# Kernel optimization log

Measured on AMD Instinct MI355X. Metric: run time of the kernel, lower is better.

## Reference

```python
import jax, jax.numpy as jnp
from jax import lax
import numpy as np

# sym6 reconstruction low-pass (pywt Wavelet('sym6').filter_bank[2]), length 12
SYM6_REC = [-0.007800708325034148, 0.0017677118642428036, 0.04472490177066578,
            -0.021060292512300564, -0.07263752278646252, 0.3379294217276218,
            0.787641141030194, 0.4910559419267466, -0.048311742585633,
            -0.11799011114819057, 0.0034907120842174702, 0.015404109327027373]

UP, DOWN = 1, 2
PAD = (len(SYM6_REC) - UP) // 2  # = 5


def setup_inputs() -> dict:
    key = jax.random.key(0)
    h = jnp.asarray(SYM6_REC, dtype=jnp.float32)
    kernel = h[None, :] * h[:, None]  # [12, 12] separable outer product
    x = jax.random.normal(key, (16, 64, 256, 256), dtype=jnp.float32)
    return {"input": x, "kernel": kernel}


def reference(input, kernel):
    # upfirdn2d: zero-insert upsample (lhs_dilation), pad, FIR convolve
    # (true convolution => flip kernel for lax correlation), strided downsample.
    B, C, H, W = input.shape
    w = jnp.flip(kernel, (0, 1))[None, None]        # [1, 1, kh, kw]
    x = input.reshape(B * C, 1, H, W)               # depthwise via batch fold
    y = lax.conv_general_dilated(
        x, w,
        window_strides=(DOWN, DOWN),
        padding=[(PAD, PAD), (PAD, PAD)],
        lhs_dilation=(UP, UP),
        dimension_numbers=('NCHW', 'OIHW', 'NCHW'))
    return y.reshape(B, C, y.shape[-2], y.shape[-1])
```

## Files before the change

kernel.cpp:

```cpp
#include <hip/hip_runtime.h>


#define H_IN  256
#define W_IN  256
#define H_OUT 128
#define W_OUT 128
#define KTAP  12
#define OTR   32
#define OTC   64
#define VSTR  148
#define NTHR  192

typedef float f32x4 __attribute__((ext_vector_type(4)));

__global__ __launch_bounds__(NTHR)
void upfirdn2d_sym6(const float* __restrict__ x,
                    const float* __restrict__ k2d,
                    float* __restrict__ out) {
    __shared__ float vs[OTR * VSTR];
    __shared__ float ks[KTAP * KTAP];
    __shared__ float wsh[KTAP];

    const int tid = threadIdx.x;

    if (tid < KTAP * KTAP) ks[tid] = k2d[tid];
    __syncthreads();
    if (tid < KTAP) {
        float tot = 0.f;
        #pragma unroll
        for (int i = 0; i < KTAP * KTAP; ++i) tot += ks[i];
        float rs = 0.f;
        #pragma unroll
        for (int q = 0; q < KTAP; ++q) rs += ks[(KTAP - 1 - tid) * KTAP + q];
        wsh[tid] = rs * rsqrtf(tot);
    }
    __syncthreads();
    float w[KTAP];
    #pragma unroll
    for (int p = 0; p < KTAP; ++p) w[p] = wsh[p];

    const int img = blockIdx.y;
    const int ti  = blockIdx.x >> 1;
    const int tj  = blockIdx.x & 1;
    const float* xim = x + (size_t)img * (H_IN * W_IN);

    const int gc0 = 128 * tj - 8;
    const bool edge_rows = (ti == 0) || (ti == 3);

    if (tid < 144) {
        const int rg  = tid / 36;
        const int cg  = tid - rg * 36;
        const int col = gc0 + 4 * cg;
        const bool colok = (unsigned)col < (unsigned)W_IN;
        const int i0  = rg * 8;
        const int gr0 = 64 * ti + 16 * rg - 5;

        float4 acc[8];
        #pragma unroll
        for (int k = 0; k < 8; ++k) acc[k] = make_float4(0.f, 0.f, 0.f, 0.f);

        if (!edge_rows) {
            const float* rp = xim + (size_t)gr0 * W_IN + col;
            #pragma unroll
            for (int rr = 0; rr < 26; ++rr) {
                float4 v = make_float4(0.f, 0.f, 0.f, 0.f);
                if (colok) v = *reinterpret_cast<const float4*>(rp);
                rp += W_IN;
                #pragma unroll
                for (int ri = 0; ri < 8; ++ri) {
                    const int p = rr - 2 * ri;
                    if (p >= 0 && p < KTAP) {
                        acc[ri].x = fmaf(w[p], v.x, acc[ri].x);
                        acc[ri].y = fmaf(w[p], v.y, acc[ri].y);
                        acc[ri].z = fmaf(w[p], v.z, acc[ri].z);
                        acc[ri].w = fmaf(w[p], v.w, acc[ri].w);
                    }
                }
            }
        } else {
            #pragma unroll
            for (int rr = 0; rr < 26; ++rr) {
                const int gr = gr0 + rr;
                float4 v = make_float4(0.f, 0.f, 0.f, 0.f);
                if (colok && (unsigned)gr < (unsigned)H_IN)
                    v = *reinterpret_cast<const float4*>(xim + gr * W_IN + col);
                #pragma unroll
                for (int ri = 0; ri < 8; ++ri) {
                    const int p = rr - 2 * ri;
                    if (p >= 0 && p < KTAP) {
                        acc[ri].x = fmaf(w[p], v.x, acc[ri].x);
                        acc[ri].y = fmaf(w[p], v.y, acc[ri].y);
                        acc[ri].z = fmaf(w[p], v.z, acc[ri].z);
                        acc[ri].w = fmaf(w[p], v.w, acc[ri].w);
                    }
                }
            }
        }
        #pragma unroll
        for (int ri = 0; ri < 8; ++ri)
            *reinterpret_cast<float4*>(&vs[(i0 + ri) * VSTR + 4 * cg]) = acc[ri];
    }
    __syncthreads();

    float* oim = out + (size_t)img * (H_OUT * W_OUT);
    for (int t = tid; t < 256; t += NTHR) {
        const int i = t >> 3;
        const int g = t & 7;

        float f[32];
        #pragma unroll
        for (int m = 0; m < 8; ++m) {
            float4 v4 = *reinterpret_cast<const float4*>(&vs[i * VSTR + 16 * g + 4 * m]);
            f[4*m+0] = v4.x; f[4*m+1] = v4.y; f[4*m+2] = v4.z; f[4*m+3] = v4.w;
        }
        float o[8];
        #pragma unroll
        for (int jj = 0; jj < 8; ++jj) {
            float a = 0.f;
            #pragma unroll
            for (int q = 0; q < KTAP; ++q)
                a = fmaf(w[q], f[2*jj + 3 + q], a);
            o[jj] = a;
        }
        const int orow = ti * OTR + i;
        const int ocol = tj * OTC + 8 * g;
        f32x4 o0 = { o[0], o[1], o[2], o[3] };
        f32x4 o1 = { o[4], o[5], o[6], o[7] };
        __builtin_nontemporal_store(o0, reinterpret_cast<f32x4*>(oim + orow * W_OUT + ocol));
        __builtin_nontemporal_store(o1, reinterpret_cast<f32x4*>(oim + orow * W_OUT + ocol + 4));
    }
}

extern "C" void kernel_launch(void* const* d_in, const int* in_sizes, int n_in,
                              void* d_out, int out_size, void* d_ws, size_t ws_size,
                              hipStream_t stream) {
    const float* x   = (const float*)d_in[0];
    const float* k2d = (const float*)d_in[1];
    float* out       = (float*)d_out;

    dim3 grid(8, 1024);
    dim3 block(NTHR);
    upfirdn2d_sym6<<<grid, block, 0, stream>>>(x, k2d, out);
}
```

Measured before the change: 70.95 us.

## Process two row tiles per block with double-buffered LDS overlap

Each block now handles two vertically adjacent 32-row output tiles, halving the grid. The second tile's vertical pass runs before the first tile's horizontal pass, using two LDS buffers, so global loads can overlap with the shuffle-and-FMA work. This amortizes the per-block kernel-weight setup, but doubles LDS per block, which may reduce occupancy. The kernel is already close to memory-bound.

Result: no change. 69.95 us, median of 2 (-1.4%).

```diff
diff --git a/kernel.cpp b/kernel.cpp
--- a/kernel.cpp
+++ b/kernel.cpp
@@ -7,59 +7,29 @@
 #define W_OUT 128
 #define KTAP  12
 #define OTR   32
-#define OTC   64
 #define VSTR  148
 #define NTHR  192
 
 typedef float f32x4 __attribute__((ext_vector_type(4)));
 
-__global__ __launch_bounds__(NTHR)
-void upfirdn2d_sym6(const float* __restrict__ x,
-                    const float* __restrict__ k2d,
-                    float* __restrict__ out) {
-    __shared__ float vs[OTR * VSTR];
-    __shared__ float ks[KTAP * KTAP];
-    __shared__ float wsh[KTAP];
-
-    const int tid = threadIdx.x;
-
-    if (tid < KTAP * KTAP) ks[tid] = k2d[tid];
-    __syncthreads();
-    if (tid < KTAP) {
-        float tot = 0.f;
-        #pragma unroll
-        for (int i = 0; i < KTAP * KTAP; ++i) tot += ks[i];
-        float rs = 0.f;
-        #pragma unroll
-        for (int q = 0; q < KTAP; ++q) rs += ks[(KTAP - 1 - tid) * KTAP + q];
-        wsh[tid] = rs * rsqrtf(tot);
-    }
-    __syncthreads();
-    float w[KTAP];
-    #pragma unroll
-    for (int p = 0; p < KTAP; ++p) w[p] = wsh[p];
-
-    const int img = blockIdx.y;
-    const int ti  = blockIdx.x >> 1;
-    const int tj  = blockIdx.x & 1;
-    const float* xim = x + (size_t)img * (H_IN * W_IN);
-
-    const int gc0 = 128 * tj - 8;
-    const bool edge_rows = (ti == 0) || (ti == 3);
-
+__device__ __forceinline__ void vpass(const float* __restrict__ xim,
+                                      float* __restrict__ buf,
+                                      const float (&w)[KTAP],
+                                      int tid, int b ,
+                                      int gc0, bool edge) {
     if (tid < 144) {
         const int rg  = tid / 36;
         const int cg  = tid - rg * 36;
         const int col = gc0 + 4 * cg;
         const bool colok = (unsigned)col < (unsigned)W_IN;
         const int i0  = rg * 8;
-        const int gr0 = 64 * ti + 16 * rg - 5;
+        const int gr0 = 2 * (b + i0) - 5;
 
         float4 acc[8];
         #pragma unroll
         for (int k = 0; k < 8; ++k) acc[k] = make_float4(0.f, 0.f, 0.f, 0.f);
 
-        if (!edge_rows) {
+        if (!edge) {
             const float* rp = xim + (size_t)gr0 * W_IN + col;
             #pragma unroll
             for (int rr = 0; rr < 26; ++rr) {
@@ -98,11 +68,14 @@
         }
         #pragma unroll
         for (int ri = 0; ri < 8; ++ri)
-            *reinterpret_cast<float4*>(&vs[(i0 + ri) * VSTR + 4 * cg]) = acc[ri];
+            *reinterpret_cast<float4*>(&buf[(i0 + ri) * VSTR + 4 * cg]) = acc[ri];
     }
-    __syncthreads();
+}
 
-    float* oim = out + (size_t)img * (H_OUT * W_OUT);
+__device__ __forceinline__ void hpass(const float* __restrict__ buf,
+                                      const float (&w)[KTAP],
+                                      float* __restrict__ oim,
+                                      int tid, int b, int ocol0) {
     for (int t = tid; t < 256; t += NTHR) {
         const int i = t >> 3;
         const int g = t & 7;
@@ -110,7 +83,7 @@
         float f[32];
         #pragma unroll
         for (int m = 0; m < 8; ++m) {
-            float4 v4 = *reinterpret_cast<const float4*>(&vs[i * VSTR + 16 * g + 4 * m]);
+            float4 v4 = *reinterpret_cast<const float4*>(&buf[i * VSTR + 16 * g + 4 * m]);
             f[4*m+0] = v4.x; f[4*m+1] = v4.y; f[4*m+2] = v4.z; f[4*m+3] = v4.w;
         }
         float o[8];
@@ -122,13 +95,59 @@
                 a = fmaf(w[q], f[2*jj + 3 + q], a);
             o[jj] = a;
         }
-        const int orow = ti * OTR + i;
-        const int ocol = tj * OTC + 8 * g;
         f32x4 o0 = { o[0], o[1], o[2], o[3] };
         f32x4 o1 = { o[4], o[5], o[6], o[7] };
-        __builtin_nontemporal_store(o0, reinterpret_cast<f32x4*>(oim + orow * W_OUT + ocol));
-        __builtin_nontemporal_store(o1, reinterpret_cast<f32x4*>(oim + orow * W_OUT + ocol + 4));
+        float* dst = oim + (size_t)(b + i) * W_OUT + ocol0 + 8 * g;
+        __builtin_nontemporal_store(o0, reinterpret_cast<f32x4*>(dst));
+        __builtin_nontemporal_store(o1, reinterpret_cast<f32x4*>(dst + 4));
     }
+}
+
+__global__ __launch_bounds__(NTHR)
+void upfirdn2d_sym6(const float* __restrict__ x,
+                    const float* __restrict__ k2d,
+                    float* __restrict__ out) {
+    __shared__ float vs[2][OTR * VSTR];
+    __shared__ float ks[KTAP * KTAP];
+    __shared__ float wsh[KTAP];
+
+    const int tid = threadIdx.x;
+
+    if (tid < KTAP * KTAP) ks[tid] = k2d[tid];
+    __syncthreads();
+    if (tid < KTAP) {
+        float tot = 0.f;
+        #pragma unroll
+        for (int i = 0; i < KTAP * KTAP; ++i) tot += ks[i];
+        float rs = 0.f;
+        #pragma unroll
+        for (int q = 0; q < KTAP; ++q) rs += ks[(KTAP - 1 - tid) * KTAP + q];
+        wsh[tid] = rs * rsqrtf(tot);
+    }
+    __syncthreads();
+    float w[KTAP];
+    #pragma unroll
+    for (int p = 0; p < KTAP; ++p) w[p] = wsh[p];
+
+    const int img = blockIdx.y;
+    const int ti  = blockIdx.x >> 1;
+    const int tj  = blockIdx.x & 1;
+    const float* xim = x + (size_t)img * (H_IN * W_IN);
+    float* oim = out + (size_t)img * (H_OUT * W_OUT);
+
+    const int gc0 = 128 * tj - 8;
+    const int b0  = 64 * ti;
+    const int b1  = 64 * ti + 32;
+    const bool e0 = (ti == 0);
+    const bool e1 = (ti == 1);
+    const int ocol0 = 64 * tj;
+
+    vpass(xim, vs[0], w, tid, b0, gc0, e0);
+    __syncthreads();
+    vpass(xim, vs[1], w, tid, b1, gc0, e1);
+    hpass(vs[0], w, oim, tid, b0, ocol0);
+    __syncthreads();
+    hpass(vs[1], w, oim, tid, b1, ocol0);
 }
 
 extern "C" void kernel_launch(void* const* d_in, const int* in_sizes, int n_in,
@@ -138,7 +157,7 @@
     const float* k2d = (const float*)d_in[1];
     float* out       = (float*)d_out;
 
-    dim3 grid(8, 1024);
+    dim3 grid(4, 1024);
     dim3 block(NTHR);
     upfirdn2d_sym6<<<grid, block, 0, stream>>>(x, k2d, out);
 }
```

## Make blocks persistent over images and streamline separable weight setup

Applied to the files above, without the earlier changes.

The grid shrinks from 1024 to 256 image rows of blocks, and each block now loops over four images, so the filter-weight setup is paid once per block instead of once per image. The weight derivation now has 12 threads read the kernel rows as float4 and write row sums to shared memory, and every thread computes the total and normalised weights itself. This removes one barrier and the 144-element shared staging. The trade-off is fewer resident blocks to hide memory latency, plus an extra barrier per image iteration.

After: 73.20 us. +3.2%, slower.

```diff
diff --git a/kernel.cpp b/kernel.cpp
--- a/kernel.cpp
+++ b/kernel.cpp
@@ -10,6 +10,8 @@
 #define OTC   64
 #define VSTR  148
 #define NTHR  192
+#define NIMG  1024
+#define IMG_STRIDE 256
 
 typedef float f32x4 __attribute__((ext_vector_type(4)));
 
@@ -18,116 +20,120 @@
                     const float* __restrict__ k2d,
                     float* __restrict__ out) {
     __shared__ float vs[OTR * VSTR];
-    __shared__ float ks[KTAP * KTAP];
-    __shared__ float wsh[KTAP];
+    __shared__ float rsum[KTAP];
 
     const int tid = threadIdx.x;
 
-    if (tid < KTAP * KTAP) ks[tid] = k2d[tid];
-    __syncthreads();
     if (tid < KTAP) {
-        float tot = 0.f;
-        #pragma unroll
-        for (int i = 0; i < KTAP * KTAP; ++i) tot += ks[i];
-        float rs = 0.f;
-        #pragma unroll
-        for (int q = 0; q < KTAP; ++q) rs += ks[(KTAP - 1 - tid) * KTAP + q];
-        wsh[tid] = rs * rsqrtf(tot);
+        const float4* kp = reinterpret_cast<const float4*>(k2d + 12 * tid);
+        float4 a = kp[0], b = kp[1], c = kp[2];
+        rsum[tid] = ((a.x + a.y) + (a.z + a.w))
+                  + ((b.x + b.y) + (b.z + b.w))
+                  + ((c.x + c.y) + (c.z + c.w));
     }
     __syncthreads();
     float w[KTAP];
-    #pragma unroll
-    for (int p = 0; p < KTAP; ++p) w[p] = wsh[p];
+    {
+        float tot = 0.f;
+        #pragma unroll
+        for (int q = 0; q < KTAP; ++q) tot += rsum[q];
+        const float r = rsqrtf(tot);
+        #pragma unroll
+        for (int p = 0; p < KTAP; ++p) w[p] = rsum[KTAP - 1 - p] * r;
+    }
 
-    const int img = blockIdx.y;
     const int ti  = blockIdx.x >> 1;
     const int tj  = blockIdx.x & 1;
-    const float* xim = x + (size_t)img * (H_IN * W_IN);
-
     const int gc0 = 128 * tj - 8;
     const bool edge_rows = (ti == 0) || (ti == 3);
 
-    if (tid < 144) {
-        const int rg  = tid / 36;
-        const int cg  = tid - rg * 36;
-        const int col = gc0 + 4 * cg;
-        const bool colok = (unsigned)col < (unsigned)W_IN;
-        const int i0  = rg * 8;
-        const int gr0 = 64 * ti + 16 * rg - 5;
+    const int rg  = tid / 36;
+    const int cg  = tid - rg * 36;
+    const int col = gc0 + 4 * cg;
+    const bool colok = (unsigned)col < (unsigned)W_IN;
+    const int i0  = rg * 8;
+    const int gr0 = 64 * ti + 16 * rg - 5;
 
-        float4 acc[8];
-        #pragma unroll
-        for (int k = 0; k < 8; ++k) acc[k] = make_float4(0.f, 0.f, 0.f, 0.f);
+    for (int img = blockIdx.y; img < NIMG; img += IMG_STRIDE) {
+        const float* xim = x + (size_t)img * (H_IN * W_IN);
+        float* oim = out + (size_t)img * (H_OUT * W_OUT);
 
-        if (!edge_rows) {
-            const float* rp = xim + (size_t)gr0 * W_IN + col;
+        if (tid < 144) {
+            float4 acc[8];
             #pragma unroll
-            for (int rr = 0; rr < 26; ++rr) {
-                float4 v = make_float4(0.f, 0.f, 0.f, 0.f);
-                if (colok) v = *reinterpret_cast<const float4*>(rp);
-                rp += W_IN;
+            for (int k = 0; k < 8; ++k) acc[k] = make_float4(0.f, 0.f, 0.f, 0.f);
+
+            if (!edge_rows) {
+                const float* rp = xim + (size_t)gr0 * W_IN + col;
                 #pragma unroll
-                for (int ri = 0; ri < 8; ++ri) {
-                    const int p = rr - 2 * ri;
-                    if (p >= 0 && p < KTAP) {
-                        acc[ri].x = fmaf(w[p], v.x, acc[ri].x);
-                        acc[ri].y = fmaf(w[p], v.y, acc[ri].y);
-                        acc[ri].z = fmaf(w[p], v.z, acc[ri].z);
-                        acc[ri].w = fmaf(w[p], v.w, acc[ri].w);
+                for (int rr = 0; rr < 26; ++rr) {
+                    float4 v = make_float4(0.f, 0.f, 0.f, 0.f);
+                    if (colok) v = *reinterpret_cast<const float4*>(rp);
+                    rp += W_IN;
+                    #pragma unroll
+                    for (int ri = 0; ri < 8; ++ri) {
+                        const int p = rr - 2 * ri;
+                        if (p >= 0 && p < KTAP) {
+                            acc[ri].x = fmaf(w[p], v.x, acc[ri].x);
+                            acc[ri].y = fmaf(w[p], v.y, acc[ri].y);
+                            acc[ri].z = fmaf(w[p], v.z, acc[ri].z);
+                            acc[ri].w = fmaf(w[p], v.w, acc[ri].w);
+                        }
+                    }
+                }
+            } else {
+                #pragma unroll
+                for (int rr = 0; rr < 26; ++rr) {
+                    const int gr = gr0 + rr;
+                    float4 v = make_float4(0.f, 0.f, 0.f, 0.f);
+                    if (colok && (unsigned)gr < (unsigned)H_IN)
+                        v = *reinterpret_cast<const float4*>(xim + gr * W_IN + col);
+                    #pragma unroll
+                    for (int ri = 0; ri < 8; ++ri) {
+                        const int p = rr - 2 * ri;
+                        if (p >= 0 && p < KTAP) {
+                            acc[ri].x = fmaf(w[p], v.x, acc[ri].x);
+                            acc[ri].y = fmaf(w[p], v.y, acc[ri].y);
+                            acc[ri].z = fmaf(w[p], v.z, acc[ri].z);
+                            acc[ri].w = fmaf(w[p], v.w, acc[ri].w);
+                        }
                     }
                 }
             }
-        } else {
             #pragma unroll
-            for (int rr = 0; rr < 26; ++rr) {
-                const int gr = gr0 + rr;
-                float4 v = make_float4(0.f, 0.f, 0.f, 0.f);
-                if (colok && (unsigned)gr < (unsigned)H_IN)
-                    v = *reinterpret_cast<const float4*>(xim + gr * W_IN + col);
+            for (int ri = 0; ri < 8; ++ri)
+                *reinterpret_cast<float4*>(&vs[(i0 + ri) * VSTR + 4 * cg]) = acc[ri];
+        }
+        __syncthreads();
+
+        for (int t = tid; t < 256; t += NTHR) {
+            const int i = t >> 3;
+            const int g = t & 7;
+
+            float f[32];
+            #pragma unroll
+            for (int m = 0; m < 8; ++m) {
+                float4 v4 = *reinterpret_cast<const float4*>(&vs[i * VSTR + 16 * g + 4 * m]);
+                f[4*m+0] = v4.x; f[4*m+1] = v4.y; f[4*m+2] = v4.z; f[4*m+3] = v4.w;
+            }
+            float o[8];
+            #pragma unroll
+            for (int jj = 0; jj < 8; ++jj) {
+                float a = 0.f;
                 #pragma unroll
-                for (int ri = 0; ri < 8; ++ri) {
-                    const int p = rr - 2 * ri;
-                    if (p >= 0 && p < KTAP) {
-                        acc[ri].x = fmaf(w[p], v.x, acc[ri].x);
-                        acc[ri].y = fmaf(w[p], v.y, acc[ri].y);
-                        acc[ri].z = fmaf(w[p], v.z, acc[ri].z);
-                        acc[ri].w = fmaf(w[p], v.w, acc[ri].w);
-                    }
-                }
+                for (int q = 0; q < KTAP; ++q)
+                    a = fmaf(w[q], f[2*jj + 3 + q], a);
+                o[jj] = a;
             }
+            const int orow = ti * OTR + i;
+            const int ocol = tj * OTC + 8 * g;
+            f32x4 o0 = { o[0], o[1], o[2], o[3] };
+            f32x4 o1 = { o[4], o[5], o[6], o[7] };
+            float* dst = oim + (size_t)orow * W_OUT + ocol;
+            __builtin_nontemporal_store(o0, reinterpret_cast<f32x4*>(dst));
+            __builtin_nontemporal_store(o1, reinterpret_cast<f32x4*>(dst + 4));
         }
-        #pragma unroll
-        for (int ri = 0; ri < 8; ++ri)
-            *reinterpret_cast<float4*>(&vs[(i0 + ri) * VSTR + 4 * cg]) = acc[ri];
-    }
-    __syncthreads();
-
-    float* oim = out + (size_t)img * (H_OUT * W_OUT);
-    for (int t = tid; t < 256; t += NTHR) {
-        const int i = t >> 3;
-        const int g = t & 7;
-
-        float f[32];
-        #pragma unroll
-        for (int m = 0; m < 8; ++m) {
-            float4 v4 = *reinterpret_cast<const float4*>(&vs[i * VSTR + 16 * g + 4 * m]);
-            f[4*m+0] = v4.x; f[4*m+1] = v4.y; f[4*m+2] = v4.z; f[4*m+3] = v4.w;
-        }
-        float o[8];
-        #pragma unroll
-        for (int jj = 0; jj < 8; ++jj) {
-            float a = 0.f;
-            #pragma unroll
-            for (int q = 0; q < KTAP; ++q)
-                a = fmaf(w[q], f[2*jj + 3 + q], a);
-            o[jj] = a;
-        }
-        const int orow = ti * OTR + i;
-        const int ocol = tj * OTC + 8 * g;
-        f32x4 o0 = { o[0], o[1], o[2], o[3] };
-        f32x4 o1 = { o[4], o[5], o[6], o[7] };
-        __builtin_nontemporal_store(o0, reinterpret_cast<f32x4*>(oim + orow * W_OUT + ocol));
-        __builtin_nontemporal_store(o1, reinterpret_cast<f32x4*>(oim + orow * W_OUT + ocol + 4));
+        __syncthreads();
     }
 }
 
@@ -138,7 +144,7 @@
     const float* k2d = (const float*)d_in[1];
     float* out       = (float*)d_out;
 
-    dim3 grid(8, 1024);
+    dim3 grid(8, IMG_STRIDE);
     dim3 block(NTHR);
     upfirdn2d_sym6<<<grid, block, 0, stream>>>(x, k2d, out);
 }
```
